# Performance work log

Hardware: AMD Instinct MI355X
Metric: run time of the kernel (lower is better)

Reference implementation:

```python
import jax, jax.numpy as jnp
import numpy as np

B, T, D = 32, 512, 1024
HOP, HID = 8, 350
NEG = jnp.float32(-1e30)  # stand-in for -inf in masked softmax (grad-safe)


def setup_inputs() -> dict:
    key = jax.random.key(0)
    ks = jax.random.split(key, 8)
    s = lambda k, sh, sc: (jax.random.normal(k, sh, jnp.float32) * sc)
    return {
        "input": jax.random.normal(ks[0], (B, T, D), jnp.float32),
        "lg": T,  # unused by the module's forward, kept for signature fidelity
        "W0": s(ks[1], (D, 3 * D), 0.02),
        "b0": jnp.zeros((2 * D,), jnp.float32),
        "W1": s(ks[2], (D, 3 * D), 0.02),
        "b1": jnp.zeros((2 * D,), jnp.float32),
        "ws1": s(ks[3], (HID, D), 0.02),
        "ws2": s(ks[4], (HOP, HID), 0.02),
        "fc_w": s(ks[5], (D, HOP * D), 0.02),
        "fc_b": jnp.zeros((D,), jnp.float32),
    }


def sru_layer(x, W, b):
    # x: [T, B, d]; SRU with use_tanh=True, identity highway (d_in == d_out).
    d = W.shape[1] // 3
    U = jnp.einsum('tbi,ij->tbj', x, W)            # one big GEMM for all gates
    xt = U[..., :d]
    f = jax.nn.sigmoid(U[..., d:2 * d] + b[:d])    # forget gate
    r = jax.nn.sigmoid(U[..., 2 * d:] + b[d:])     # reset/highway gate

    def step(c, u):
        xt_t, f_t = u
        c = f_t * c + (1.0 - f_t) * xt_t
        return c, c

    c0 = jnp.zeros(xt.shape[1:], xt.dtype)
    _, cs = jax.lax.scan(step, c0, (xt, f))        # elementwise gated recurrence
    return r * jnp.tanh(cs) + (1.0 - r) * x


def reference(input, lg, W0, b0, W1, b1, ws1, ws2, fc_w, fc_b):
    # lengths per _process_lengths: T - count of positions where feature-0 == 0
    lengths = T - jnp.sum((input[:, :, 0] == 0).astype(jnp.int32), axis=1)  # [B]

    x = jnp.transpose(input, (1, 0, 2))            # [T, B, D]
    x = sru_layer(x, W0, b0)
    x = sru_layer(x, W1, b1)
    x = jnp.transpose(x, (1, 0, 2))                # [B, T, D]

    # multi-hop self-attention pooling (dropout is identity in eval mode)
    hbar = jnp.tanh(jnp.einsum('btd,hd->bth', x, ws1))   # [B, T, HID]
    alphas = jnp.einsum('bth,kh->bkt', hbar, ws2)        # [B, HOP, T]
    mask = jnp.arange(T)[None, None, :] >= lengths[:, None, None]
    attn = jax.nn.softmax(jnp.where(mask, NEG, alphas), axis=2)  # [B, HOP, T]

    pooled = jnp.einsum('bkt,btd->bkd', attn, x).reshape(input.shape[0], -1)
    out = pooled @ fc_w.T + fc_b                   # [B, D]
    return out, attn
```

## Files before the change

### kernel.cpp

```cpp
#include <hip/hip_runtime.h>
#include <hip/hip_bf16.h>

#define B_ 32
#define T_ 512
#define D_ 1024
#define HOP_ 8
#define HID_ 350
#define NEGV -1e30f
#define CH_ 4

typedef __bf16 v8bf __attribute__((ext_vector_type(8)));
typedef float  v4f  __attribute__((ext_vector_type(4)));

__device__ __forceinline__ float fast_sigmoid(float x) {
    return 1.0f / (1.0f + __expf(-x));
}
__device__ __forceinline__ float fast_tanh(float x) {
    return 1.0f - 2.0f / (__expf(2.0f * x) + 1.0f);
}
__device__ __forceinline__ float bf2f(unsigned short u) {
    unsigned x = ((unsigned)u) << 16;
    float f;
    __builtin_memcpy(&f, &x, 4);
    return f;
}
__device__ __forceinline__ unsigned short f2bf(float v) {
    __hip_bfloat16 h = __float2bfloat16(v);
    unsigned short u;
    __builtin_memcpy(&u, &h, 2);
    return u;
}

__global__ __launch_bounds__(512) void lengths_k(const float* __restrict__ input,
                                                 int* __restrict__ len) {
    int b = blockIdx.x;
    int t = threadIdx.x;
    int z = (input[((size_t)b * T_ + t) * D_] == 0.0f) ? 1 : 0;
    __shared__ int cnt;
    if (t == 0) cnt = 0;
    __syncthreads();
    unsigned long long m = __ballot(z);
    if ((t & 63) == 0) atomicAdd(&cnt, __popcll(m));
    __syncthreads();
    if (t == 0) len[b] = T_ - cnt;
}


__global__ __launch_bounds__(256) void convX_k(const float* __restrict__ in,
                                               unsigned short* __restrict__ out) {
    int i = (blockIdx.x * 256 + threadIdx.x) * 4;
    float4 v = *(const float4*)&in[i];
    out[i + 0] = f2bf(v.x);
    out[i + 1] = f2bf(v.y);
    out[i + 2] = f2bf(v.z);
    out[i + 3] = f2bf(v.w);
}

template <bool NT>
__global__ __launch_bounds__(256) void convW_k(const float* __restrict__ W,
                                               unsigned short* __restrict__ Wp,
                                               int K, int N, int nT, int Nreal) {
    int o = blockIdx.x * 256 + threadIdx.x;
    int tile = o >> 12;
    int within = o & 4095;
    int n_l = within >> 5, k_l = within & 31;
    int kb = tile / nT, nbb = tile % nT;
    int n = nbb * 128 + n_l, k = kb * 32 + k_l;
    float v = 0.f;
    if (NT) {
        if (n < Nreal) v = W[(size_t)n * K + k];
    } else {
        v = W[(size_t)k * N + n];
    }
    Wp[o] = f2bf(v);
}

template <int EPI>
__global__ __launch_bounds__(256) void gemm_mfma(
    const unsigned short* __restrict__ A,
    const unsigned short* __restrict__ Bp,
    const float* __restrict__ bias,
    void* __restrict__ C,
    int K, int nT, int Nstore) {
    __shared__ __align__(16) unsigned short As[128 * 32];
    __shared__ __align__(16) unsigned short Bs[128 * 32];
    const int tid = threadIdx.x;
    const int lane = tid & 63;
    const int wid = __builtin_amdgcn_readfirstlane(tid >> 6);
    const int wm = wid & 1, wn = wid >> 1;
    const int m0 = blockIdx.y * 128;
    const int n0 = blockIdx.x * 128;
    const int nb = blockIdx.x;
    const int quad = lane >> 4;
    const int l15 = lane & 15;

    v4f acc[4][4];
#pragma unroll
    for (int i = 0; i < 4; ++i)
#pragma unroll
        for (int j = 0; j < 4; ++j) acc[i][j] = (v4f)(0.f);

    const int nKB = K >> 5;
    for (int kb = 0; kb < nKB; ++kb) {
        __syncthreads();
#pragma unroll
        for (int p = 0; p < 2; ++p) {
            int g = p * 256 + wid * 64 + lane;
            const unsigned short* gp = A + (size_t)(m0 + (g >> 2)) * K + kb * 32 + (g & 3) * 8;
            int ldsOff = (p * 256 + wid * 64) * 16;
            __builtin_amdgcn_global_load_lds(
                (const __attribute__((address_space(1))) void*)gp,
                (__attribute__((address_space(3))) void*)((char*)As + ldsOff),
                16, 0, 0);
        }
        const unsigned short* bt = Bp + (size_t)(kb * nT + nb) * (128 * 32);
#pragma unroll
        for (int p = 0; p < 2; ++p) {
            int g = p * 256 + wid * 64 + lane;
            const unsigned short* gp = bt + g * 8;
            int ldsOff = (p * 256 + wid * 64) * 16;
            __builtin_amdgcn_global_load_lds(
                (const __attribute__((address_space(1))) void*)gp,
                (__attribute__((address_space(3))) void*)((char*)Bs + ldsOff),
                16, 0, 0);
        }
        __syncthreads();
        v8bf af[4], bfr[4];
#pragma unroll
        for (int mi = 0; mi < 4; ++mi)
            af[mi] = *(const v8bf*)&As[(wm * 64 + mi * 16 + l15) * 32 + quad * 8];
#pragma unroll
        for (int ni = 0; ni < 4; ++ni)
            bfr[ni] = *(const v8bf*)&Bs[(wn * 64 + ni * 16 + l15) * 32 + quad * 8];
#pragma unroll
        for (int mi = 0; mi < 4; ++mi)
#pragma unroll
            for (int ni = 0; ni < 4; ++ni)
                acc[mi][ni] = __builtin_amdgcn_mfma_f32_16x16x32_bf16(
                    af[mi], bfr[ni], acc[mi][ni], 0, 0, 0);
    }

    const int baseM = m0 + wm * 64;
    const int baseN = n0 + wn * 64;
    if (EPI == 0) {
        unsigned short* Up = (unsigned short*)C;
#pragma unroll
        for (int ni = 0; ni < 4; ++ni) {
            int j = baseN + ni * 16 + l15;
            bool sig = j >= 1024;
            float bv = sig ? bias[j - 1024] : 0.f;
#pragma unroll
            for (int mi = 0; mi < 4; ++mi) {
                int m = baseM + mi * 16 + quad * 4;
                v4f c = acc[mi][ni];
#pragma unroll
                for (int r = 0; r < 4; ++r) {
                    float v = c[r];
                    if (sig) v = fast_sigmoid(v + bv);
                    Up[(size_t)(m + r) * 3072 + j] = f2bf(v);
                }
            }
        }
    } else {
        float* Cf = (float*)C;
#pragma unroll
        for (int ni = 0; ni < 4; ++ni) {
            int j = baseN + ni * 16 + l15;
            if (j < Nstore) {
#pragma unroll
                for (int mi = 0; mi < 4; ++mi) {
                    int m = baseM + mi * 16 + quad * 4;
                    v4f c = acc[mi][ni];
#pragma unroll
                    for (int r = 0; r < 4; ++r)
                        Cf[(size_t)(m + r) * Nstore + j] = fast_tanh(c[r]);
                }
            }
        }
    }
}

#define LOADG(T0, XT, F, R, XV)                                          \
    _Pragma("unroll") for (int j = 0; j < 8; ++j) {                      \
        const unsigned short* u = Ub + (size_t)((T0) + j) * 3072;        \
        XT[j] = bf2f(u[0]);                                              \
        F[j] = bf2f(u[1024]);                                            \
        R[j] = bf2f(u[2048]);                                            \
        XV[j] = RESF32 ? xrf[(size_t)((T0) + j) * D_]                    \
                       : bf2f(xrb[(size_t)((T0) + j) * D_]);             \
    }
#define STEP8(T0, XT, F, R, XV)                                          \
    _Pragma("unroll") for (int j = 0; j < 8; ++j) {                      \
        c = F[j] * c + (1.f - F[j]) * XT[j];                             \
        float o = R[j] * fast_tanh(c) + (1.f - R[j]) * XV[j];            \
        ob[(size_t)((T0) + j) * D_] = f2bf(o);                           \
    }

template <bool RESF32>
__global__ __launch_bounds__(64) void sru_scan_bf(const unsigned short* __restrict__ Up,
                                                  const float* __restrict__ xresf,
                                                  const unsigned short* __restrict__ xresb,
                                                  unsigned short* __restrict__ xoutb) {
    int idx = blockIdx.x * 64 + threadIdx.x;
    int b = idx >> 10, d = idx & (D_ - 1);
    const unsigned short* Ub = Up + (size_t)b * T_ * 3072 + d;
    const float* xrf = RESF32 ? (xresf + (size_t)b * T_ * D_ + d) : nullptr;
    const unsigned short* xrb = RESF32 ? nullptr : (xresb + (size_t)b * T_ * D_ + d);
    unsigned short* ob = xoutb + (size_t)b * T_ * D_ + d;
    float c = 0.f;
    float axt[8], afv[8], arv[8], axv[8];
    float bxt[8], bfv[8], brv[8], bxv[8];
    LOADG(0, axt, afv, arv, axv);
    for (int t0 = 0; t0 < T_; t0 += 16) {
        LOADG(t0 + 8, bxt, bfv, brv, bxv);
        STEP8(t0, axt, afv, arv, axv);
        if (t0 + 16 < T_) { LOADG(t0 + 16, axt, afv, arv, axv); }
        STEP8(t0 + 8, bxt, bfv, brv, bxv);
    }
}


template <bool BT, bool DO_TANH>
__global__ __launch_bounds__(256) void gemm64(const float* __restrict__ A,
                                              const float* __restrict__ Bm,
                                              float* __restrict__ C,
                                              int M, int N, int K) {
    __shared__ float Asm[16][64];
    __shared__ float Bsm[16][64];
    const int tid = threadIdx.x;
    const int tx = tid & 15;
    const int ty = tid >> 4;
    const int m0 = blockIdx.y * 64;
    const int n0 = blockIdx.x * 64;
    float acc[4][4] = {};
    const int ar = tid >> 2;
    const int ac = (tid & 3) << 2;

    for (int k0 = 0; k0 < K; k0 += 16) {
        {
            float4 v = *(const float4*)&A[(size_t)(m0 + ar) * K + k0 + ac];
            Asm[ac + 0][ar] = v.x; Asm[ac + 1][ar] = v.y;
            Asm[ac + 2][ar] = v.z; Asm[ac + 3][ar] = v.w;
        }
        if (!BT) {
            int kk = tid >> 4;
            int c4 = (tid & 15) << 2;
            float4 v = *(const float4*)&Bm[(size_t)(k0 + kk) * N + n0 + c4];
            Bsm[kk][c4 + 0] = v.x; Bsm[kk][c4 + 1] = v.y;
            Bsm[kk][c4 + 2] = v.z; Bsm[kk][c4 + 3] = v.w;
        } else {
            int nn = tid >> 2;
            int kk = (tid & 3) << 2;
            int row = n0 + nn;
            if (row < N) {
                float4 v = *(const float4*)&Bm[(size_t)row * K + k0 + kk];
                Bsm[kk + 0][nn] = v.x; Bsm[kk + 1][nn] = v.y;
                Bsm[kk + 2][nn] = v.z; Bsm[kk + 3][nn] = v.w;
            } else {
                Bsm[kk + 0][nn] = 0.f; Bsm[kk + 1][nn] = 0.f;
                Bsm[kk + 2][nn] = 0.f; Bsm[kk + 3][nn] = 0.f;
            }
        }
        __syncthreads();
#pragma unroll
        for (int kk = 0; kk < 16; ++kk) {
            float4 a = *(const float4*)&Asm[kk][ty << 2];
            float4 b = *(const float4*)&Bsm[kk][tx << 2];
            float am[4] = {a.x, a.y, a.z, a.w};
            float bm[4] = {b.x, b.y, b.z, b.w};
#pragma unroll
            for (int i = 0; i < 4; ++i)
#pragma unroll
                for (int j = 0; j < 4; ++j)
                    acc[i][j] += am[i] * bm[j];
        }
        __syncthreads();
    }
#pragma unroll
    for (int i = 0; i < 4; ++i) {
        int row = m0 + (ty << 2) + i;
#pragma unroll
        for (int j = 0; j < 4; ++j) {
            int col = n0 + (tx << 2) + j;
            if (col < N) {
                float v = acc[i][j];
                if (DO_TANH) v = fast_tanh(v);
                C[(size_t)row * N + col] = v;
            }
        }
    }
}

__global__ __launch_bounds__(256) void sru_scan(const float* __restrict__ U,
                                                const float* __restrict__ bias,
                                                const float* __restrict__ xin,
                                                float* __restrict__ xout) {
    int idx = blockIdx.x * 256 + threadIdx.x;
    int b = idx >> 10;
    int d = idx & (D_ - 1);
    float bfv = bias[d], br = bias[D_ + d];
    float c = 0.0f;
    const float* Ub = U + (size_t)b * T_ * (3 * D_);
    const float* xb = xin + (size_t)b * T_ * D_;
    float* ob = xout + (size_t)b * T_ * D_;
    for (int t = 0; t < T_; t += 8) {
        float ux[8], uf[8], ur[8], xv[8];
#pragma unroll
        for (int j = 0; j < 8; ++j) {
            const float* u = Ub + (size_t)(t + j) * (3 * D_);
            ux[j] = u[d];
            uf[j] = u[D_ + d];
            ur[j] = u[2 * D_ + d];
            xv[j] = xb[(size_t)(t + j) * D_ + d];
        }
#pragma unroll
        for (int j = 0; j < 8; ++j) {
            float f = fast_sigmoid(uf[j] + bfv);
            float r = fast_sigmoid(ur[j] + br);
            c = f * c + (1.0f - f) * ux[j];
            ob[(size_t)(t + j) * D_ + d] = r * fast_tanh(c) + (1.0f - r) * xv[j];
        }
    }
}


__global__ __launch_bounds__(256) void alphas_k(const float* __restrict__ hbar,
                                                const float* __restrict__ ws2,
                                                float* __restrict__ alph) {
    __shared__ float w[HOP_][352];
    for (int i = threadIdx.x; i < HOP_ * HID_; i += 256)
        w[i / HID_][i % HID_] = ws2[i];
    __syncthreads();
    int bt = blockIdx.x * 256 + threadIdx.x;
    const float* hr = hbar + (size_t)bt * HID_;
    float acc[HOP_] = {};
    for (int h = 0; h < HID_; ++h) {
        float hv = hr[h];
#pragma unroll
        for (int k = 0; k < HOP_; ++k) acc[k] += w[k][h] * hv;
    }
    float* ar = alph + (size_t)bt * HOP_;
#pragma unroll
    for (int k = 0; k < HOP_; ++k) ar[k] = acc[k];
}

__global__ __launch_bounds__(256) void softmax_k(const float* __restrict__ alph,
                                                 const int* __restrict__ len,
                                                 float* __restrict__ attn) {
    int b = blockIdx.x >> 3, k = blockIdx.x & 7;
    int L = len[b];
    int t0 = threadIdx.x, t1 = threadIdx.x + 256;
    float v0 = (t0 >= L) ? NEGV : alph[((size_t)b * T_ + t0) * HOP_ + k];
    float v1 = (t1 >= L) ? NEGV : alph[((size_t)b * T_ + t1) * HOP_ + k];
    __shared__ float redm[4];
    __shared__ float reds[4];
    float m = fmaxf(v0, v1);
#pragma unroll
    for (int off = 32; off; off >>= 1) m = fmaxf(m, __shfl_xor(m, off));
    if ((threadIdx.x & 63) == 0) redm[threadIdx.x >> 6] = m;
    __syncthreads();
    m = fmaxf(fmaxf(redm[0], redm[1]), fmaxf(redm[2], redm[3]));
    float e0 = __expf(v0 - m), e1 = __expf(v1 - m);
    float s = e0 + e1;
#pragma unroll
    for (int off = 32; off; off >>= 1) s += __shfl_xor(s, off);
    if ((threadIdx.x & 63) == 0) reds[threadIdx.x >> 6] = s;
    __syncthreads();
    s = reds[0] + reds[1] + reds[2] + reds[3];
    float inv = 1.0f / s;
    float* ar = attn + ((size_t)b * HOP_ + k) * T_;
    ar[t0] = e0 * inv;
    ar[t1] = e1 * inv;
}

__global__ __launch_bounds__(256) void pooled_bf_k(const float* __restrict__ attn,
                                                   const unsigned short* __restrict__ x2b,
                                                   float* __restrict__ pooled) {
    __shared__ float at[HOP_][T_];
    int b = blockIdx.x >> 2;
    int d0 = (blockIdx.x & 3) * 256;
    for (int i = threadIdx.x; i < HOP_ * T_; i += 256)
        at[i >> 9][i & (T_ - 1)] = attn[(size_t)b * HOP_ * T_ + i];
    __syncthreads();
    int d = d0 + threadIdx.x;
    float acc[HOP_] = {};
    const unsigned short* xb = x2b + (size_t)b * T_ * D_ + d;
    for (int t = 0; t < T_; ++t) {
        float xv = bf2f(xb[(size_t)t * D_]);
#pragma unroll
        for (int k = 0; k < HOP_; ++k) acc[k] += at[k][t] * xv;
    }
#pragma unroll
    for (int k = 0; k < HOP_; ++k)
        pooled[((size_t)b * HOP_ + k) * D_ + d] = acc[k];
}

__global__ __launch_bounds__(256) void pooled_k(const float* __restrict__ attn,
                                                const float* __restrict__ x2,
                                                float* __restrict__ pooled) {
    __shared__ float at[HOP_][T_];
    int b = blockIdx.x >> 2;
    int d0 = (blockIdx.x & 3) * 256;
    for (int i = threadIdx.x; i < HOP_ * T_; i += 256)
        at[i >> 9][i & (T_ - 1)] = attn[(size_t)b * HOP_ * T_ + i];
    __syncthreads();
    int d = d0 + threadIdx.x;
    float acc[HOP_] = {};
    const float* xb = x2 + (size_t)b * T_ * D_ + d;
    for (int t = 0; t < T_; ++t) {
        float xv = xb[(size_t)t * D_];
#pragma unroll
        for (int k = 0; k < HOP_; ++k) acc[k] += at[k][t] * xv;
    }
#pragma unroll
    for (int k = 0; k < HOP_; ++k)
        pooled[((size_t)b * HOP_ + k) * D_ + d] = acc[k];
}

__global__ __launch_bounds__(256) void fc_k(const float* __restrict__ pooled,
                                            const float* __restrict__ fcw,
                                            const float* __restrict__ fcb,
                                            float* __restrict__ out) {
    __shared__ float w[8][1028];
    int j0 = blockIdx.x * 8;
    int b = threadIdx.x >> 3, jj = threadIdx.x & 7;
    float acc = 0.0f;
    for (int p0 = 0; p0 < HOP_ * D_; p0 += 1024) {
        __syncthreads();
        for (int i = threadIdx.x * 4; i < 8 * 1024; i += 256 * 4) {
            int r = i >> 10, c = i & 1023;
            *(float4*)&w[r][c] = *(const float4*)&fcw[(size_t)(j0 + r) * (HOP_ * D_) + p0 + c];
        }
        __syncthreads();
        const float* pr = pooled + (size_t)b * (HOP_ * D_) + p0;
#pragma unroll 4
        for (int i = 0; i < 1024; i += 4) {
            float4 wv = *(const float4*)&w[jj][i];
            float4 pv = *(const float4*)&pr[i];
            acc += wv.x * pv.x + wv.y * pv.y + wv.z * pv.z + wv.w * pv.w;
        }
    }
    out[(size_t)b * D_ + j0 + jj] = acc + fcb[j0 + jj];
}

extern "C" void kernel_launch(void* const* d_in, const int* in_sizes, int n_in,
                              void* d_out, int out_size, void* d_ws, size_t ws_size,
                              hipStream_t stream) {
    const float* input = (const float*)d_in[0];
    const float* W0   = (const float*)d_in[2];
    const float* b0   = (const float*)d_in[3];
    const float* W1   = (const float*)d_in[4];
    const float* b1   = (const float*)d_in[5];
    const float* ws1  = (const float*)d_in[6];
    const float* ws2  = (const float*)d_in[7];
    const float* fc_w = (const float*)d_in[8];
    const float* fc_b = (const float*)d_in[9];

    float* out  = (float*)d_out;
    float* attn = out + (size_t)B_ * D_;
    (void)in_sizes; (void)n_in; (void)out_size;

    const int M = B_ * T_;
    char* ws = (char*)d_ws;

    const size_t NEED_A = 181141632ull;
    const size_t NEED_B = 80478336ull;
    const size_t NEED_FB = 100663424ull;

    if (ws_size >= NEED_B) {
        const int CHv = (ws_size >= NEED_A) ? 32 : 8;
        const size_t szU = (size_t)CHv * 512 * 3072 * 2;
        const size_t szX = (size_t)CHv * 512 * 1024 * 2;
        unsigned short* Uc   = (unsigned short*)ws;
        unsigned short* xbc  = (unsigned short*)(ws + szU);
        unsigned short* x2b  = (unsigned short*)(ws + szU + szX);
        unsigned short* W0p  = (unsigned short*)(ws + szU + szX + 33554432);
        unsigned short* W1p  = W0p + 3145728;
        unsigned short* ws1p = W1p + 3145728;
        int*            len  = (int*)(ws1p + 393216);
        float* hbar   = (float*)ws;
        float* alph   = (float*)(ws + 22937600);
        float* pooled = (float*)(ws + 23461888);

        lengths_k<<<B_, 512, 0, stream>>>(input, len);
        convW_k<false><<<(D_ * 3 * D_) / 256, 256, 0, stream>>>(W0, W0p, D_, 3 * D_, 24, 3 * D_);
        convW_k<false><<<(D_ * 3 * D_) / 256, 256, 0, stream>>>(W1, W1p, D_, 3 * D_, 24, 3 * D_);
        convW_k<true><<<(D_ * 384) / 256, 256, 0, stream>>>(ws1, ws1p, D_, 384, 3, HID_);

        for (int c0 = 0; c0 < B_; c0 += CHv) {
            const float* inC = input + (size_t)c0 * T_ * D_;
            const int Mc = CHv * T_;
            convX_k<<<(Mc * D_ / 4) / 256, 256, 0, stream>>>(inC, xbc);
            gemm_mfma<0><<<dim3(24, Mc / 128), 256, 0, stream>>>(xbc, W0p, b0, Uc, D_, 24, 0);
            sru_scan_bf<true><<<CHv * D_ / 64, 64, 0, stream>>>(Uc, inC, nullptr, xbc);
            gemm_mfma<0><<<dim3(24, Mc / 128), 256, 0, stream>>>(xbc, W1p, b1, Uc, D_, 24, 0);
            sru_scan_bf<false><<<CHv * D_ / 64, 64, 0, stream>>>(
                Uc, nullptr, xbc, x2b + (size_t)c0 * T_ * D_);
        }

        gemm_mfma<1><<<dim3(3, M / 128), 256, 0, stream>>>(x2b, ws1p, nullptr, hbar, D_, 3, HID_);

        alphas_k<<<M / 256, 256, 0, stream>>>(hbar, ws2, alph);
        softmax_k<<<B_ * HOP_, 256, 0, stream>>>(alph, len, attn);
        pooled_bf_k<<<B_ * 4, 256, 0, stream>>>(attn, x2b, pooled);
        fc_k<<<D_ / 8, 256, 0, stream>>>(pooled, fc_w, fc_b, out);
        return;
    }

    if (ws_size < NEED_FB) return;

    float* U    = (float*)ws;
    float* x1c  = (float*)(ws + 25165824);
    float* x2   = (float*)(ws + 33554432);
    int*   len  = (int*)(ws + 100663296);
    float* hbar   = (float*)ws;
    float* alph   = (float*)(ws + 22937600);
    float* pooled = (float*)(ws + 23461888);

    lengths_k<<<B_, 512, 0, stream>>>(input, len);

    const int Mc = CH_ * T_;
    for (int c0 = 0; c0 < B_; c0 += CH_) {
        const float* inC = input + (size_t)c0 * T_ * D_;
        float* x2C = x2 + (size_t)c0 * T_ * D_;
        gemm64<false, false><<<dim3(3 * D_ / 64, Mc / 64), 256, 0, stream>>>(
            inC, W0, U, Mc, 3 * D_, D_);
        sru_scan<<<CH_ * D_ / 256, 256, 0, stream>>>(U, b0, inC, x1c);
        gemm64<false, false><<<dim3(3 * D_ / 64, Mc / 64), 256, 0, stream>>>(
            x1c, W1, U, Mc, 3 * D_, D_);
        sru_scan<<<CH_ * D_ / 256, 256, 0, stream>>>(U, b1, x1c, x2C);
    }

    gemm64<true, true><<<dim3((HID_ + 63) / 64, M / 64), 256, 0, stream>>>(
        x2, ws1, hbar, M, HID_, D_);
    alphas_k<<<M / 256, 256, 0, stream>>>(hbar, ws2, alph);
    softmax_k<<<B_ * HOP_, 256, 0, stream>>>(alph, len, attn);
    pooled_k<<<B_ * 4, 256, 0, stream>>>(attn, x2, pooled);
    fc_k<<<D_ / 8, 256, 0, stream>>>(pooled, fc_w, fc_b, out);
}
```

Baseline: 825.6 us.

## Parallelize SRU scan over time segments and stage GEMM epilogue through LDS

```diff
diff --git a/kernel.cpp b/kernel.cpp
--- a/kernel.cpp
+++ b/kernel.cpp
@@ -79,11 +79,11 @@
 __global__ __launch_bounds__(256) void gemm_mfma(
     const unsigned short* __restrict__ A,
     const unsigned short* __restrict__ Bp,
-    const float* __restrict__ bias,
     void* __restrict__ C,
     int K, int nT, int Nstore) {
-    __shared__ __align__(16) unsigned short As[128 * 32];
-    __shared__ __align__(16) unsigned short Bs[128 * 32];
+    __shared__ __align__(16) char smem[34816];
+    unsigned short* As = (unsigned short*)smem;
+    unsigned short* Bs = (unsigned short*)(smem + 8192);
     const int tid = threadIdx.x;
     const int lane = tid & 63;
     const int wid = __builtin_amdgcn_readfirstlane(tid >> 6);
@@ -140,28 +140,34 @@
                     af[mi], bfr[ni], acc[mi][ni], 0, 0, 0);
     }
 
-    const int baseM = m0 + wm * 64;
-    const int baseN = n0 + wn * 64;
     if (EPI == 0) {
-        unsigned short* Up = (unsigned short*)C;
+        __syncthreads();
+        unsigned short* Ct = (unsigned short*)smem;
 #pragma unroll
         for (int ni = 0; ni < 4; ++ni) {
-            int j = baseN + ni * 16 + l15;
-            bool sig = j >= 1024;
-            float bv = sig ? bias[j - 1024] : 0.f;
+            int n_l = wn * 64 + ni * 16 + l15;
 #pragma unroll
             for (int mi = 0; mi < 4; ++mi) {
-                int m = baseM + mi * 16 + quad * 4;
-                v4f c = acc[mi][ni];
-#pragma unroll
-                for (int r = 0; r < 4; ++r) {
-                    float v = c[r];
-                    if (sig) v = fast_sigmoid(v + bv);
-                    Up[(size_t)(m + r) * 3072 + j] = f2bf(v);
-                }
+                int m_l = wm * 64 + mi * 16 + quad * 4;
+                v4f cc = acc[mi][ni];
+#pragma unroll
+                for (int r = 0; r < 4; ++r)
+                    Ct[(m_l + r) * 136 + n_l] = f2bf(cc[r]);
             }
         }
+        __syncthreads();
+        int row = tid >> 1;
+        int colH = (tid & 1) << 6;
+        unsigned short* gdst = (unsigned short*)C + (size_t)(m0 + row) * 3072 + n0 + colH;
+        const unsigned short* lsrc = Ct + row * 136 + colH;
+#pragma unroll
+        for (int i = 0; i < 8; ++i) {
+            uint4 v = *(const uint4*)(lsrc + i * 8);
+            *(uint4*)(gdst + i * 8) = v;
+        }
     } else {
+        const int baseM = m0 + wm * 64;
+        const int baseN = n0 + wn * 64;
         float* Cf = (float*)C;
 #pragma unroll
         for (int ni = 0; ni < 4; ++ni) {
@@ -180,42 +186,70 @@
     }
 }
 
-#define LOADG(T0, XT, F, R, XV)                                          \
-    _Pragma("unroll") for (int j = 0; j < 8; ++j) {                      \
-        const unsigned short* u = Ub + (size_t)((T0) + j) * 3072;        \
-        XT[j] = bf2f(u[0]);                                              \
-        F[j] = bf2f(u[1024]);                                            \
-        R[j] = bf2f(u[2048]);                                            \
-        XV[j] = RESF32 ? xrf[(size_t)((T0) + j) * D_]                    \
-                       : bf2f(xrb[(size_t)((T0) + j) * D_]);             \
-    }
-#define STEP8(T0, XT, F, R, XV)                                          \
-    _Pragma("unroll") for (int j = 0; j < 8; ++j) {                      \
-        c = F[j] * c + (1.f - F[j]) * XT[j];                             \
-        float o = R[j] * fast_tanh(c) + (1.f - R[j]) * XV[j];            \
-        ob[(size_t)((T0) + j) * D_] = f2bf(o);                           \
-    }
-
-template <bool RESF32>
-__global__ __launch_bounds__(64) void sru_scan_bf(const unsigned short* __restrict__ Up,
-                                                  const float* __restrict__ xresf,
-                                                  const unsigned short* __restrict__ xresb,
-                                                  unsigned short* __restrict__ xoutb) {
-    int idx = blockIdx.x * 64 + threadIdx.x;
-    int b = idx >> 10, d = idx & (D_ - 1);
+__global__ __launch_bounds__(512) void sru_scan_seg(
+    const unsigned short* __restrict__ Up,
+    const float* __restrict__ bias,
+    const unsigned short* __restrict__ xres,
+    unsigned short* __restrict__ xout) {
+    int b = blockIdx.x >> 4;
+    int d0 = (blockIdx.x & 15) << 6;
+    int dl = threadIdx.x & 63;
+    int s = threadIdx.x >> 6;
+    int d = d0 + dl;
+    float bf = bias[d], br = bias[D_ + d];
     const unsigned short* Ub = Up + (size_t)b * T_ * 3072 + d;
-    const float* xrf = RESF32 ? (xresf + (size_t)b * T_ * D_ + d) : nullptr;
-    const unsigned short* xrb = RESF32 ? nullptr : (xresb + (size_t)b * T_ * D_ + d);
-    unsigned short* ob = xoutb + (size_t)b * T_ * D_ + d;
-    float c = 0.f;
-    float axt[8], afv[8], arv[8], axv[8];
-    float bxt[8], bfv[8], brv[8], bxv[8];
-    LOADG(0, axt, afv, arv, axv);
-    for (int t0 = 0; t0 < T_; t0 += 16) {
-        LOADG(t0 + 8, bxt, bfv, brv, bxv);
-        STEP8(t0, axt, afv, arv, axv);
-        if (t0 + 16 < T_) { LOADG(t0 + 16, axt, afv, arv, axv); }
-        STEP8(t0 + 8, bxt, bfv, brv, bxv);
+    const int t0 = s * 64;
+
+    float Aa = 1.f, Bv = 0.f;
+    for (int tt = 0; tt < 64; tt += 8) {
+        float xt[8], fv[8];
+#pragma unroll
+        for (int j = 0; j < 8; ++j) {
+            const unsigned short* u = Ub + (size_t)(t0 + tt + j) * 3072;
+            xt[j] = bf2f(u[0]);
+            fv[j] = bf2f(u[1024]);
+        }
+#pragma unroll
+        for (int j = 0; j < 8; ++j) {
+            float f = fast_sigmoid(fv[j] + bf);
+            Aa *= f;
+            Bv = f * Bv + (1.f - f) * xt[j];
+        }
+    }
+    __shared__ float Asm[8][64], Bsm[8][64], cinS[8][64];
+    Asm[s][dl] = Aa;
+    Bsm[s][dl] = Bv;
+    __syncthreads();
+    if (threadIdx.x < 64) {
+        float c = 0.f;
+#pragma unroll
+        for (int ss = 0; ss < 8; ++ss) {
+            cinS[ss][threadIdx.x] = c;
+            c = Asm[ss][threadIdx.x] * c + Bsm[ss][threadIdx.x];
+        }
+    }
+    __syncthreads();
+    float c = cinS[s][dl];
+    const unsigned short* xr = xres + (size_t)b * T_ * D_ + d;
+    unsigned short* ob = xout + (size_t)b * T_ * D_ + d;
+    for (int tt = 0; tt < 64; tt += 4) {
+        float xt[4], fv[4], rv[4], xv[4];
+#pragma unroll
+        for (int j = 0; j < 4; ++j) {
+            const unsigned short* u = Ub + (size_t)(t0 + tt + j) * 3072;
+            xt[j] = bf2f(u[0]);
+            fv[j] = bf2f(u[1024]);
+            rv[j] = bf2f(u[2048]);
+            xv[j] = bf2f(xr[(size_t)(t0 + tt + j) * D_]);
+        }
+#pragma unroll
+        for (int j = 0; j < 4; ++j) {
+            float f = fast_sigmoid(fv[j] + bf);
+            float r = fast_sigmoid(rv[j] + br);
+            c = f * c + (1.f - f) * xt[j];
+            float o = r * fast_tanh(c) + (1.f - r) * xv[j];
+            ob[(size_t)(t0 + tt + j) * D_] = f2bf(o);
+        }
     }
 }
 
@@ -491,14 +525,14 @@
             const float* inC = input + (size_t)c0 * T_ * D_;
             const int Mc = CHv * T_;
             convX_k<<<(Mc * D_ / 4) / 256, 256, 0, stream>>>(inC, xbc);
-            gemm_mfma<0><<<dim3(24, Mc / 128), 256, 0, stream>>>(xbc, W0p, b0, Uc, D_, 24, 0);
-            sru_scan_bf<true><<<CHv * D_ / 64, 64, 0, stream>>>(Uc, inC, nullptr, xbc);
-            gemm_mfma<0><<<dim3(24, Mc / 128), 256, 0, stream>>>(xbc, W1p, b1, Uc, D_, 24, 0);
-            sru_scan_bf<false><<<CHv * D_ / 64, 64, 0, stream>>>(
-                Uc, nullptr, xbc, x2b + (size_t)c0 * T_ * D_);
-        }
-
-        gemm_mfma<1><<<dim3(3, M / 128), 256, 0, stream>>>(x2b, ws1p, nullptr, hbar, D_, 3, HID_);
+            gemm_mfma<0><<<dim3(24, Mc / 128), 256, 0, stream>>>(xbc, W0p, Uc, D_, 24, 0);
+            sru_scan_seg<<<CHv * 16, 512, 0, stream>>>(Uc, b0, xbc, xbc);
+            gemm_mfma<0><<<dim3(24, Mc / 128), 256, 0, stream>>>(xbc, W1p, Uc, D_, 24, 0);
+            sru_scan_seg<<<CHv * 16, 512, 0, stream>>>(
+                Uc, b1, xbc, x2b + (size_t)c0 * T_ * D_);
+        }
+
+        gemm_mfma<1><<<dim3(3, M / 128), 256, 0, stream>>>(x2b, ws1p, hbar, D_, 3, HID_);
 
         alphas_k<<<M / 256, 256, 0, stream>>>(hbar, ws2, alph);
         softmax_k<<<B_ * HOP_, 256, 0, stream>>>(alph, len, attn);
```

Result: faster. 781.6 us (-5.3%).
